# Performance work log

Measured on AMD Instinct MI355X. Metric: run time of the kernel, lower is better.

Reference implementation:

```python
import jax, jax.numpy as jnp
import numpy as np

B, S, D = 1, 4096, 1024
H, HKV, HD = 16, 4, 64          # q heads, kv heads, head dim
ROPE_THETA = 1e6


def setup_inputs() -> dict:
    key = jax.random.key(0)
    k1, k2, k3 = jax.random.split(key, 3)
    x = jax.random.normal(k1, (B, S, D), dtype=jnp.float32)
    # deterministic RoPE tables: pos_cis = exp(i * t * theta^{-2j/hd})
    inv_freq = 1.0 / (ROPE_THETA ** (np.arange(0, HD, 2, dtype=np.float32) / HD))  # [HD//2]
    ang = np.arange(S, dtype=np.float32)[:, None] * inv_freq[None, :]              # [S, HD//2]
    pos_cos = jnp.asarray(np.cos(ang), dtype=jnp.float32)
    pos_sin = jnp.asarray(np.sin(ang), dtype=jnp.float32)
    w_qkv = jax.random.normal(k2, (D, (H + 2 * HKV) * HD), dtype=jnp.float32) * 0.02
    w_o = jax.random.normal(k3, (H * HD, D), dtype=jnp.float32) * 0.02
    return {"x": x, "pos_cos": pos_cos, "pos_sin": pos_sin, "w_qkv": w_qkv, "w_o": w_o}


def _rope(t, pos_cos, pos_sin):
    # t: [B, S, h, HD]; complex pairs are consecutive elements on last dim
    te, to = t[..., 0::2], t[..., 1::2]
    cos = pos_cos[None, :, None, :]
    sin = pos_sin[None, :, None, :]
    oe = te * cos - to * sin
    oo = te * sin + to * cos
    return jnp.stack([oe, oo], axis=-1).reshape(t.shape)


def reference(x, pos_cos, pos_sin, w_qkv, w_o):
    qkv = jnp.einsum("bsd,de->bse", x, w_qkv)  # fused QKV projection
    q = qkv[..., : H * HD].reshape(B, S, H, HD)
    k = qkv[..., H * HD : (H + HKV) * HD].reshape(B, S, HKV, HD)
    v = qkv[..., (H + HKV) * HD :].reshape(B, S, HKV, HD)
    q = _rope(q, pos_cos, pos_sin)
    k = _rope(k, pos_cos, pos_sin)
    # GQA: repeat kv heads to match q heads
    n_rep = H // HKV
    k = jnp.repeat(k, n_rep, axis=2)  # [B, S, H, HD]
    v = jnp.repeat(v, n_rep, axis=2)
    scale = 1.0 / jnp.sqrt(jnp.float32(HD))
    scores = jnp.einsum("bqhd,bkhd->bhqk", q, k) * scale  # [B, H, S, S]
    causal = jnp.tril(jnp.ones((S, S), dtype=bool))
    scores = jnp.where(causal[None, None], scores, jnp.float32(-1e9))
    attn = jax.nn.softmax(scores, axis=-1)
    out = jnp.einsum("bhqk,bkhd->bqhd", attn, v).reshape(B, S, H * HD)
    return jnp.einsum("bse,ed->bsd", out, w_o)
```

## Files before the change

kernel.cpp:

```cpp
#include <hip/hip_runtime.h>

#define S_LEN 4096
#define DMODEL 1024
#define NH 16
#define NKV 4
#define HDIM 64
#define NQKV 1536

typedef __attribute__((ext_vector_type(8))) short bfrag8;
typedef __attribute__((ext_vector_type(4))) float f32x4_t;

__device__ __forceinline__ unsigned short f2bf(float f) {
  unsigned int u = __builtin_bit_cast(unsigned int, f);
  return (unsigned short)((u + 0x7fffu + ((u >> 16) & 1u)) >> 16);
}

__device__ __forceinline__ unsigned int cvtpk_bf16(float lo, float hi) {
  unsigned int r;
  asm("v_cvt_pk_bf16_f32 %0, %1, %2" : "=v"(r) : "v"(lo), "v"(hi));
  return r;
}

__device__ __forceinline__ float fexp2(float x) {
  float r;
  asm("v_exp_f32 %0, %1" : "=v"(r) : "v"(x));
  return r;
}

__device__ __forceinline__ float fmax3(float a, float b, float c) {
  float r;
  asm("v_max3_f32 %0, %1, %2, %3" : "=v"(r) : "v"(a), "v"(b), "v"(c));
  return r;
}

typedef __attribute__((address_space(3))) unsigned char lds_uc;
typedef const __attribute__((address_space(1))) unsigned char glob_uc;
__device__ __forceinline__ void gl16(const void* g, void* l) {
  __builtin_amdgcn_global_load_lds((glob_uc*)g, (lds_uc*)l, 16, 0, 0);
}

__global__ void convert_bf16(const float* __restrict__ in, unsigned short* __restrict__ out, int n) {
  int idx = (blockIdx.x * 256 + threadIdx.x) * 4;
  if (idx < n) {
    float4 v = *reinterpret_cast<const float4*>(in + idx);
    out[idx + 0] = f2bf(v.x);
    out[idx + 1] = f2bf(v.y);
    out[idx + 2] = f2bf(v.z);
    out[idx + 3] = f2bf(v.w);
  }
}

__global__ void transpose_convert(const float* __restrict__ in, int ldin, long in_zstride,
                                  unsigned short* __restrict__ out, int ldout, long out_zstride,
                                  int R, int C) {
  __shared__ float tile[32][33];
  const float* inb = in + (size_t)blockIdx.z * in_zstride;
  unsigned short* outb = out + (size_t)blockIdx.z * out_zstride;
  int c0 = blockIdx.x * 32, r0 = blockIdx.y * 32;
  int tx = threadIdx.x, ty = threadIdx.y;
  for (int i = 0; i < 4; ++i) {
    int r = r0 + ty + i * 8;
    tile[ty + i * 8][tx] = inb[(size_t)r * ldin + c0 + tx];
  }
  __syncthreads();
  for (int i = 0; i < 4; ++i) {
    int c = c0 + ty + i * 8;
    outb[(size_t)c * ldout + r0 + tx] = f2bf(tile[tx][ty + i * 8]);
  }
}

__global__ void rope_kernel(const float* __restrict__ qkv,
                            const float* __restrict__ pcos, const float* __restrict__ psin,
                            unsigned short* __restrict__ Qh, unsigned short* __restrict__ Kh) {
  const float SCL = 0.125f * 1.44269504f;
  int s = blockIdx.x;
  int t = threadIdx.x;
  const float* row = qkv + (size_t)s * NQKV;
  for (int p = t; p < 640; p += 256) {
    int i = p & 31;
    float c = pcos[s * 32 + i], sn = psin[s * 32 + i];
    if (p < 512) {
      int h = p >> 5;
      float te = row[h * 64 + 2 * i], to = row[h * 64 + 2 * i + 1];
      size_t base = ((size_t)h * S_LEN + s) * 64;
      Qh[base + 2 * i]     = f2bf((te * c - to * sn) * SCL);
      Qh[base + 2 * i + 1] = f2bf((te * sn + to * c) * SCL);
    } else {
      int hk = (p - 512) >> 5;
      float te = row[1024 + hk * 64 + 2 * i], to = row[1024 + hk * 64 + 2 * i + 1];
      size_t base = ((size_t)hk * S_LEN + s) * 64;
      Kh[base + 2 * i]     = f2bf(te * c - to * sn);
      Kh[base + 2 * i + 1] = f2bf(te * sn + to * c);
    }
  }
}

__global__ __launch_bounds__(256) void gemm_bf16(
    const unsigned short* __restrict__ A,
    const unsigned short* __restrict__ Bt,
    float* __restrict__ C, int M, int N, int K) {
  __shared__ __align__(16) unsigned short As[128 * 32];
  __shared__ __align__(16) unsigned short Bs[128 * 32];
  int m0 = blockIdx.x * 128, n0 = blockIdx.y * 128;
  int t = threadIdx.x, lane = t & 63, wid = t >> 6;
  int wm = (wid >> 1) * 64, wn = (wid & 1) * 64;
  int fr = lane & 15, kb = lane >> 4;
  int srow = t >> 2, scol = (t & 3) * 8;
  const unsigned short* Ag0 = A + (size_t)(m0 + srow) * K + scol;
  const unsigned short* Ag1 = A + (size_t)(m0 + 64 + srow) * K + scol;
  const unsigned short* Bg0 = Bt + (size_t)(n0 + srow) * K + scol;
  const unsigned short* Bg1 = Bt + (size_t)(n0 + 64 + srow) * K + scol;
  char* AsW0 = (char*)As + wid * 1024;
  char* AsW1 = (char*)As + 4096 + wid * 1024;
  char* BsW0 = (char*)Bs + wid * 1024;
  char* BsW1 = (char*)Bs + 4096 + wid * 1024;

  f32x4_t acc[4][4];
#pragma unroll
  for (int r = 0; r < 4; ++r)
#pragma unroll
    for (int c = 0; c < 4; ++c) acc[r][c] = (f32x4_t){0.f, 0.f, 0.f, 0.f};

  for (int k0 = 0; k0 < K; k0 += 32) {
    __syncthreads();
    gl16(Ag0 + k0, AsW0);
    gl16(Ag1 + k0, AsW1);
    gl16(Bg0 + k0, BsW0);
    gl16(Bg1 + k0, BsW1);
    __syncthreads();
    bfrag8 af[4], bfr[4];
#pragma unroll
    for (int rb = 0; rb < 4; ++rb)
      af[rb] = *reinterpret_cast<const bfrag8*>(&As[(wm + rb * 16 + fr) * 32 + kb * 8]);
#pragma unroll
    for (int cb = 0; cb < 4; ++cb)
      bfr[cb] = *reinterpret_cast<const bfrag8*>(&Bs[(wn + cb * 16 + fr) * 32 + kb * 8]);
#pragma unroll
    for (int rb = 0; rb < 4; ++rb)
#pragma unroll
      for (int cb = 0; cb < 4; ++cb)
        acc[rb][cb] = __builtin_amdgcn_mfma_f32_16x16x32_bf16(af[rb], bfr[cb], acc[rb][cb], 0, 0, 0);
  }
  int rowg = (lane >> 4) * 4, colg = lane & 15;
#pragma unroll
  for (int rb = 0; rb < 4; ++rb)
#pragma unroll
    for (int cb = 0; cb < 4; ++cb)
#pragma unroll
      for (int j = 0; j < 4; ++j) {
        int r = m0 + wm + rb * 16 + rowg + j;
        int c = n0 + wn + cb * 16 + colg;
        C[(size_t)r * N + c] = acc[rb][cb][j];
      }
}

__global__ __launch_bounds__(256) void flash_attn(
    const unsigned short* __restrict__ Qh,
    const unsigned short* __restrict__ Kh,
    const unsigned short* __restrict__ Vt,
    unsigned short* __restrict__ aout) {
  __shared__ __align__(16) char SMEM[18432];
  int bid = blockIdx.x;
  int head = bid & 15, hk = head >> 2;
  int qt = 127 - (bid >> 4);
  int qrow0 = qt * 32;
  int t = threadIdx.x, lane = t & 63, wid = t >> 6;
  int fr = lane & 15, kb = lane >> 4, rloc = kb * 4;
  char* Pw = SMEM + wid * 4096;
  int swz = (fr & 7) << 4;

  const unsigned short* Qbase = Qh + ((size_t)head * S_LEN + qrow0) * 64;
  bfrag8 qf[2][2];
  qf[0][0] = *reinterpret_cast<const bfrag8*>(Qbase + fr * 64 + kb * 8);
  qf[0][1] = *reinterpret_cast<const bfrag8*>(Qbase + fr * 64 + 32 + kb * 8);
  qf[1][0] = *reinterpret_cast<const bfrag8*>(Qbase + (16 + fr) * 64 + kb * 8);
  qf[1][1] = *reinterpret_cast<const bfrag8*>(Qbase + (16 + fr) * 64 + 32 + kb * 8);

  const unsigned short* Kt = Kh + (size_t)hk * S_LEN * 64;
  const unsigned short* Vb = Vt + (size_t)hk * 64 * S_LEN;
  int koff = fr * 64 + kb * 8;
  int voff = fr * S_LEN + kb * 8;

  float m_r[2] = {-1e30f, -1e30f}, l_r[2] = {0.f, 0.f};
  f32x4_t acc[2][4];
#pragma unroll
  for (int g = 0; g < 2; ++g)
#pragma unroll
    for (int dt = 0; dt < 4; ++dt) acc[g][dt] = (f32x4_t){0.f, 0.f, 0.f, 0.f};

  int ntt = (qrow0 + 95) / 64;
  int nf = (qrow0 >= 63) ? ((qrow0 - 63) / 64 + 1) : 0;
  int c0 = (wid * ntt) >> 2, c1 = ((wid + 1) * ntt) >> 2;

  if (c0 < c1) {
    bfrag8 kf[4][2];
    {
      const unsigned short* K0 = Kt + c0 * 64 * 64 + koff;
#pragma unroll
      for (int ct = 0; ct < 4; ++ct) {
        kf[ct][0] = *reinterpret_cast<const bfrag8*>(K0 + ct * 1024);
        kf[ct][1] = *reinterpret_cast<const bfrag8*>(K0 + ct * 1024 + 32);
      }
    }
    for (int kt = c0; kt < c1; ++kt) {
      int kv0 = kt * 64;
      const unsigned short* Vtile = Vb + kv0 + voff;
      bfrag8 vf[2][4];
#pragma unroll
      for (int hh = 0; hh < 2; ++hh)
#pragma unroll
        for (int dt = 0; dt < 4; ++dt)
          vf[hh][dt] = *reinterpret_cast<const bfrag8*>(Vtile + dt * 16 * S_LEN + hh * 32);
      __builtin_amdgcn_sched_barrier(0);
      f32x4_t sc[2][4];
      __builtin_amdgcn_s_setprio(1);
#pragma unroll
      for (int ct = 0; ct < 4; ++ct) {
        f32x4_t z0 = (f32x4_t){0.f, 0.f, 0.f, 0.f};
        z0 = __builtin_amdgcn_mfma_f32_16x16x32_bf16(kf[ct][0], qf[0][0], z0, 0, 0, 0);
        sc[0][ct] = __builtin_amdgcn_mfma_f32_16x16x32_bf16(kf[ct][1], qf[0][1], z0, 0, 0, 0);
        f32x4_t z1 = (f32x4_t){0.f, 0.f, 0.f, 0.f};
        z1 = __builtin_amdgcn_mfma_f32_16x16x32_bf16(kf[ct][0], qf[1][0], z1, 0, 0, 0);
        sc[1][ct] = __builtin_amdgcn_mfma_f32_16x16x32_bf16(kf[ct][1], qf[1][1], z1, 0, 0, 0);
      }
      __builtin_amdgcn_s_setprio(0);
      if (kt + 1 < c1) {
        const unsigned short* Kn = Kt + (kv0 + 64) * 64 + koff;
#pragma unroll
        for (int ct = 0; ct < 4; ++ct) {
          kf[ct][0] = *reinterpret_cast<const bfrag8*>(Kn + ct * 1024);
          kf[ct][1] = *reinterpret_cast<const bfrag8*>(Kn + ct * 1024 + 32);
        }
      }
      __builtin_amdgcn_sched_barrier(0);
      if (kt >= nf) {
#pragma unroll
        for (int g = 0; g < 2; ++g) {
          int grow = qrow0 + g * 16 + fr;
#pragma unroll
          for (int ct = 0; ct < 4; ++ct)
#pragma unroll
            for (int j = 0; j < 4; ++j)
              sc[g][ct][j] = ((kv0 + ct * 16 + kb * 4 + j) <= grow) ? sc[g][ct][j] : -1e30f;
        }
      }
      float pmax[2];
#pragma unroll
      for (int g = 0; g < 2; ++g) {
        float pm = fmax3(sc[g][0][0], sc[g][0][1], sc[g][0][2]);
        pm = fmax3(pm, sc[g][0][3], sc[g][1][0]);
        pm = fmax3(pm, sc[g][1][1], sc[g][1][2]);
        pm = fmax3(pm, sc[g][1][3], sc[g][2][0]);
        pm = fmax3(pm, sc[g][2][1], sc[g][2][2]);
        pm = fmax3(pm, sc[g][2][3], sc[g][3][0]);
        pm = fmax3(pm, sc[g][3][1], sc[g][3][2]);
        pm = fmaxf(pm, sc[g][3][3]);
        pm = fmaxf(pm, __shfl_xor(pm, 16));
        pmax[g] = fmaxf(pm, __shfl_xor(pm, 32));
      }
      bool need = (pmax[0] > m_r[0] + 8.0f) || (pmax[1] > m_r[1] + 8.0f);
      if (__any(need)) {
#pragma unroll
        for (int g = 0; g < 2; ++g) {
          float mnew = fmaxf(m_r[g], pmax[g]);
          float a = fexp2(m_r[g] - mnew);
          l_r[g] *= a;
          m_r[g] = mnew;
#pragma unroll
          for (int j = 0; j < 4; ++j) {
            float aj = __shfl(a, rloc + j);
#pragma unroll
            for (int dt = 0; dt < 4; ++dt) acc[g][dt][j] *= aj;
          }
        }
      }
#pragma unroll
      for (int g = 0; g < 2; ++g) {
        float s = 0.f;
#pragma unroll
        for (int ct = 0; ct < 4; ++ct)
#pragma unroll
          for (int j = 0; j < 4; ++j) {
            float p = fexp2(sc[g][ct][j] - m_r[g]);
            sc[g][ct][j] = p;
            s += p;
          }
        s += __shfl_xor(s, 16);
        s += __shfl_xor(s, 32);
        l_r[g] += s;
      }
#pragma unroll
      for (int g = 0; g < 2; ++g)
#pragma unroll
        for (int ct = 0; ct < 4; ++ct) {
          unsigned int u01 = cvtpk_bf16(sc[g][ct][0], sc[g][ct][1]);
          unsigned int u23 = cvtpk_bf16(sc[g][ct][2], sc[g][ct][3]);
          unsigned long long w = ((unsigned long long)u23 << 32) | u01;
          *reinterpret_cast<unsigned long long*>(
              Pw + (g * 16 + fr) * 128 + ((ct * 32 + kb * 8) ^ swz)) = w;
        }
      __builtin_amdgcn_s_setprio(1);
#pragma unroll
      for (int hh = 0; hh < 2; ++hh) {
        bfrag8 pa0 = *reinterpret_cast<const bfrag8*>(Pw + fr * 128 + ((hh * 64 + kb * 16) ^ swz));
        bfrag8 pa1 = *reinterpret_cast<const bfrag8*>(Pw + (16 + fr) * 128 + ((hh * 64 + kb * 16) ^ swz));
#pragma unroll
        for (int dt = 0; dt < 4; ++dt) {
          acc[0][dt] = __builtin_amdgcn_mfma_f32_16x16x32_bf16(pa0, vf[hh][dt], acc[0][dt], 0, 0, 0);
          acc[1][dt] = __builtin_amdgcn_mfma_f32_16x16x32_bf16(pa1, vf[hh][dt], acc[1][dt], 0, 0, 0);
        }
      }
      __builtin_amdgcn_s_setprio(0);
    }
  }

  float* stgA = (float*)SMEM;
  float* stgB = (float*)(SMEM + 9216);
  __syncthreads();
  if (wid == 1 || wid == 3) {
    float* R = (wid == 1) ? stgA : stgB;
#pragma unroll
    for (int g = 0; g < 2; ++g) {
#pragma unroll
      for (int dt = 0; dt < 4; ++dt)
#pragma unroll
        for (int j = 0; j < 4; ++j)
          R[(g * 16 + dt * 4 + j) * 64 + lane] = acc[g][dt][j];
      R[(32 + g * 2) * 64 + lane] = m_r[g];
      R[(33 + g * 2) * 64 + lane] = l_r[g];
    }
  }
  __syncthreads();
  if (wid == 0 || wid == 2) {
    float* R = (wid == 0) ? stgA : stgB;
#pragma unroll
    for (int g = 0; g < 2; ++g) {
      float mo = R[(32 + g * 2) * 64 + lane], lo = R[(33 + g * 2) * 64 + lane];
      float mm = fmaxf(m_r[g], mo);
      float ca = fexp2(m_r[g] - mm), cb = fexp2(mo - mm);
      l_r[g] = l_r[g] * ca + lo * cb;
      m_r[g] = mm;
#pragma unroll
      for (int j = 0; j < 4; ++j) {
        float caj = __shfl(ca, rloc + j);
        float cbj = __shfl(cb, rloc + j);
#pragma unroll
        for (int dt = 0; dt < 4; ++dt)
          acc[g][dt][j] = acc[g][dt][j] * caj + R[(g * 16 + dt * 4 + j) * 64 + lane] * cbj;
      }
    }
    if (wid == 2) {
#pragma unroll
      for (int g = 0; g < 2; ++g) {
#pragma unroll
        for (int dt = 0; dt < 4; ++dt)
#pragma unroll
          for (int j = 0; j < 4; ++j)
            stgB[(g * 16 + dt * 4 + j) * 64 + lane] = acc[g][dt][j];
        stgB[(32 + g * 2) * 64 + lane] = m_r[g];
        stgB[(33 + g * 2) * 64 + lane] = l_r[g];
      }
    }
  }
  __syncthreads();
  if (wid == 0) {
#pragma unroll
    for (int g = 0; g < 2; ++g) {
      float mo = stgB[(32 + g * 2) * 64 + lane], lo = stgB[(33 + g * 2) * 64 + lane];
      float mm = fmaxf(m_r[g], mo);
      float ca = fexp2(m_r[g] - mm), cb = fexp2(mo - mm);
      l_r[g] = l_r[g] * ca + lo * cb;
#pragma unroll
      for (int j = 0; j < 4; ++j) {
        float caj = __shfl(ca, rloc + j);
        float cbj = __shfl(cb, rloc + j);
#pragma unroll
        for (int dt = 0; dt < 4; ++dt)
          acc[g][dt][j] = acc[g][dt][j] * caj + stgB[(g * 16 + dt * 4 + j) * 64 + lane] * cbj;
      }
    }
#pragma unroll
    for (int g = 0; g < 2; ++g)
#pragma unroll
      for (int j = 0; j < 4; ++j) {
        float lj = __shfl(l_r[g], rloc + j);
        float inv = 1.0f / lj;
        int grow = qrow0 + g * 16 + rloc + j;
#pragma unroll
        for (int dt = 0; dt < 4; ++dt)
          aout[(size_t)grow * (NH * HDIM) + head * 64 + dt * 16 + fr] = f2bf(acc[g][dt][j] * inv);
      }
  }
}

extern "C" void kernel_launch(void* const* d_in, const int* in_sizes, int n_in,
                              void* d_out, int out_size, void* d_ws, size_t ws_size,
                              hipStream_t stream) {
  const float* x    = (const float*)d_in[0];
  const float* pcos = (const float*)d_in[1];
  const float* psin = (const float*)d_in[2];
  const float* wqkv = (const float*)d_in[3];
  const float* wo   = (const float*)d_in[4];
  float* out = (float*)d_out;

  char* ws = (char*)d_ws;
  unsigned short* xb    = (unsigned short*)ws;  ws += (size_t)S_LEN * DMODEL * 2;
  unsigned short* wqkvT = (unsigned short*)ws;  ws += (size_t)NQKV * DMODEL * 2;
  unsigned short* woT   = (unsigned short*)ws;  ws += (size_t)DMODEL * DMODEL * 2;
  float*          qkv   = (float*)ws;           ws += (size_t)S_LEN * NQKV * 4;
  unsigned short* Qh    = (unsigned short*)ws;  ws += (size_t)NH * S_LEN * HDIM * 2;
  unsigned short* Kh    = (unsigned short*)ws;  ws += (size_t)NKV * S_LEN * HDIM * 2;
  unsigned short* Vt    = (unsigned short*)ws;  ws += (size_t)NKV * HDIM * S_LEN * 2;
  unsigned short* aoutb = (unsigned short*)ws;  ws += (size_t)S_LEN * NH * HDIM * 2;

  convert_bf16<<<(S_LEN * DMODEL) / (256 * 4), 256, 0, stream>>>(x, xb, S_LEN * DMODEL);
  transpose_convert<<<dim3(NQKV / 32, DMODEL / 32, 1), dim3(32, 8), 0, stream>>>(
      wqkv, NQKV, 0, wqkvT, DMODEL, 0, DMODEL, NQKV);
  transpose_convert<<<dim3(DMODEL / 32, DMODEL / 32, 1), dim3(32, 8), 0, stream>>>(
      wo, DMODEL, 0, woT, DMODEL, 0, DMODEL, DMODEL);
  gemm_bf16<<<dim3(S_LEN / 128, NQKV / 128), 256, 0, stream>>>(xb, wqkvT, qkv, S_LEN, NQKV, DMODEL);
  rope_kernel<<<S_LEN, 256, 0, stream>>>(qkv, pcos, psin, Qh, Kh);
  transpose_convert<<<dim3(HDIM / 32, S_LEN / 32, NKV), dim3(32, 8), 0, stream>>>(
      qkv + 1280, NQKV, 64, Vt, S_LEN, (long)HDIM * S_LEN, S_LEN, HDIM);
  flash_attn<<<dim3(2048), 256, 0, stream>>>(Qh, Kh, Vt, aoutb);
  gemm_bf16<<<dim3(S_LEN / 128, DMODEL / 128), 256, 0, stream>>>(aoutb, woT, out, S_LEN, DMODEL, DMODEL);
}
```

Baseline: 204.1 us.

## Split flash-attention KV range across eight waves with tree merge

```diff
diff --git a/kernel.cpp b/kernel.cpp
--- a/kernel.cpp
+++ b/kernel.cpp
@@ -154,12 +154,12 @@
       }
 }
 
-__global__ __launch_bounds__(256) void flash_attn(
+__global__ __launch_bounds__(512) void flash_attn(
     const unsigned short* __restrict__ Qh,
     const unsigned short* __restrict__ Kh,
     const unsigned short* __restrict__ Vt,
     unsigned short* __restrict__ aout) {
-  __shared__ __align__(16) char SMEM[18432];
+  __shared__ __align__(16) char SMEM[32768 + 2048];
   int bid = blockIdx.x;
   int head = bid & 15, hk = head >> 2;
   int qt = 127 - (bid >> 4);
@@ -167,6 +167,7 @@
   int t = threadIdx.x, lane = t & 63, wid = t >> 6;
   int fr = lane & 15, kb = lane >> 4, rloc = kb * 4;
   char* Pw = SMEM + wid * 4096;
+  float* mlp = (float*)(SMEM + 32768);
   int swz = (fr & 7) << 4;
 
   const unsigned short* Qbase = Qh + ((size_t)head * S_LEN + qrow0) * 64;
@@ -190,7 +191,7 @@
 
   int ntt = (qrow0 + 95) / 64;
   int nf = (qrow0 >= 63) ? ((qrow0 - 63) / 64 + 1) : 0;
-  int c0 = (wid * ntt) >> 2, c1 = ((wid + 1) * ntt) >> 2;
+  int c0 = (wid * ntt) >> 3, c1 = ((wid + 1) * ntt) >> 3;
 
   if (c0 < c1) {
     bfrag8 kf[4][2];
@@ -314,71 +315,52 @@
     }
   }
 
-  float* stgA = (float*)SMEM;
-  float* stgB = (float*)(SMEM + 9216);
-  __syncthreads();
-  if (wid == 1 || wid == 3) {
-    float* R = (wid == 1) ? stgA : stgB;
-#pragma unroll
-    for (int g = 0; g < 2; ++g) {
-#pragma unroll
-      for (int dt = 0; dt < 4; ++dt)
-#pragma unroll
-        for (int j = 0; j < 4; ++j)
-          R[(g * 16 + dt * 4 + j) * 64 + lane] = acc[g][dt][j];
-      R[(32 + g * 2) * 64 + lane] = m_r[g];
-      R[(33 + g * 2) * 64 + lane] = l_r[g];
-    }
-  }
-  __syncthreads();
-  if (wid == 0 || wid == 2) {
-    float* R = (wid == 0) ? stgA : stgB;
-#pragma unroll
-    for (int g = 0; g < 2; ++g) {
-      float mo = R[(32 + g * 2) * 64 + lane], lo = R[(33 + g * 2) * 64 + lane];
-      float mm = fmaxf(m_r[g], mo);
-      float ca = fexp2(m_r[g] - mm), cb = fexp2(mo - mm);
-      l_r[g] = l_r[g] * ca + lo * cb;
-      m_r[g] = mm;
-#pragma unroll
-      for (int j = 0; j < 4; ++j) {
-        float caj = __shfl(ca, rloc + j);
-        float cbj = __shfl(cb, rloc + j);
-#pragma unroll
-        for (int dt = 0; dt < 4; ++dt)
-          acc[g][dt][j] = acc[g][dt][j] * caj + R[(g * 16 + dt * 4 + j) * 64 + lane] * cbj;
-      }
-    }
-    if (wid == 2) {
-#pragma unroll
-      for (int g = 0; g < 2; ++g) {
-#pragma unroll
-        for (int dt = 0; dt < 4; ++dt)
-#pragma unroll
-          for (int j = 0; j < 4; ++j)
-            stgB[(g * 16 + dt * 4 + j) * 64 + lane] = acc[g][dt][j];
-        stgB[(32 + g * 2) * 64 + lane] = m_r[g];
-        stgB[(33 + g * 2) * 64 + lane] = l_r[g];
-      }
-    }
-  }
+#define ML(w, g, which, row) mlp[(((w) * 2 + (g)) * 2 + (which)) * 16 + (row)]
+#define STORE_STATE(Rp)                                                   \
+  {                                                                       \
+    float* R = (Rp);                                                      \
+    _Pragma("unroll") for (int g = 0; g < 2; ++g) {                       \
+      _Pragma("unroll") for (int dt = 0; dt < 4; ++dt)                    \
+        _Pragma("unroll") for (int j = 0; j < 4; ++j)                     \
+          R[(g * 16 + dt * 4 + j) * 64 + lane] = acc[g][dt][j];           \
+      if (lane < 16) {                                                    \
+        ML(wid, g, 0, lane) = m_r[g];                                     \
+        ML(wid, g, 1, lane) = l_r[g];                                     \
+      }                                                                   \
+    }                                                                     \
+  }
+#define MERGE_STATE(Rp, wsrc)                                             \
+  {                                                                       \
+    float* R = (Rp);                                                      \
+    _Pragma("unroll") for (int g = 0; g < 2; ++g) {                       \
+      float mo = ML((wsrc), g, 0, fr), lo = ML((wsrc), g, 1, fr);         \
+      float mm = fmaxf(m_r[g], mo);                                       \
+      float ca = fexp2(m_r[g] - mm), cb = fexp2(mo - mm);                 \
+      l_r[g] = l_r[g] * ca + lo * cb;                                     \
+      m_r[g] = mm;                                                        \
+      _Pragma("unroll") for (int j = 0; j < 4; ++j) {                     \
+        float caj = __shfl(ca, rloc + j);                                 \
+        float cbj = __shfl(cb, rloc + j);                                 \
+        _Pragma("unroll") for (int dt = 0; dt < 4; ++dt)                  \
+          acc[g][dt][j] = acc[g][dt][j] * caj +                           \
+                          R[(g * 16 + dt * 4 + j) * 64 + lane] * cbj;     \
+      }                                                                   \
+    }                                                                     \
+  }
+
+  __syncthreads();
+  if (wid & 1) STORE_STATE((float*)(SMEM + (wid >> 1) * 8192));
+  __syncthreads();
+  if (!(wid & 1)) MERGE_STATE((float*)(SMEM + (wid >> 1) * 8192), wid + 1);
+  __syncthreads();
+  if (wid == 2 || wid == 6) STORE_STATE((float*)(SMEM + (wid >> 2) * 8192));
+  __syncthreads();
+  if (wid == 0 || wid == 4) MERGE_STATE((float*)(SMEM + (wid >> 2) * 8192), wid + 2);
+  __syncthreads();
+  if (wid == 4) STORE_STATE((float*)SMEM);
   __syncthreads();
   if (wid == 0) {
-#pragma unroll
-    for (int g = 0; g < 2; ++g) {
-      float mo = stgB[(32 + g * 2) * 64 + lane], lo = stgB[(33 + g * 2) * 64 + lane];
-      float mm = fmaxf(m_r[g], mo);
-      float ca = fexp2(m_r[g] - mm), cb = fexp2(mo - mm);
-      l_r[g] = l_r[g] * ca + lo * cb;
-#pragma unroll
-      for (int j = 0; j < 4; ++j) {
-        float caj = __shfl(ca, rloc + j);
-        float cbj = __shfl(cb, rloc + j);
-#pragma unroll
-        for (int dt = 0; dt < 4; ++dt)
-          acc[g][dt][j] = acc[g][dt][j] * caj + stgB[(g * 16 + dt * 4 + j) * 64 + lane] * cbj;
-      }
-    }
+    MERGE_STATE((float*)SMEM, 4);
 #pragma unroll
     for (int g = 0; g < 2; ++g)
 #pragma unroll
@@ -391,6 +373,9 @@
           aout[(size_t)grow * (NH * HDIM) + head * 64 + dt * 16 + fr] = f2bf(acc[g][dt][j] * inv);
       }
   }
+#undef ML
+#undef STORE_STATE
+#undef MERGE_STATE
 }
 
 extern "C" void kernel_launch(void* const* d_in, const int* in_sizes, int n_in,
@@ -422,6 +407,6 @@
   rope_kernel<<<S_LEN, 256, 0, stream>>>(qkv, pcos, psin, Qh, Kh);
   transpose_convert<<<dim3(HDIM / 32, S_LEN / 32, NKV), dim3(32, 8), 0, stream>>>(
       qkv + 1280, NQKV, 64, Vt, S_LEN, (long)HDIM * S_LEN, S_LEN, HDIM);
-  flash_attn<<<dim3(2048), 256, 0, stream>>>(Qh, Kh, Vt, aoutb);
+  flash_attn<<<dim3(2048), 512, 0, stream>>>(Qh, Kh, Vt, aoutb);
   gemm_bf16<<<dim3(S_LEN / 128, DMODEL / 128), 256, 0, stream>>>(aoutb, woT, out, S_LEN, DMODEL, DMODEL);
 }
```

Result: slower. 235.4 us (+15.4%).

## Split long causal KV ranges across two blocks and merge partials

Applied to the files above, without the earlier changes.

```diff
diff --git a/kernel.cpp b/kernel.cpp
--- a/kernel.cpp
+++ b/kernel.cpp
@@ -158,12 +158,20 @@
     const unsigned short* __restrict__ Qh,
     const unsigned short* __restrict__ Kh,
     const unsigned short* __restrict__ Vt,
-    unsigned short* __restrict__ aout) {
+    float* __restrict__ partial,
+    float* __restrict__ mlb) {
   __shared__ __align__(16) char SMEM[18432];
   int bid = blockIdx.x;
   int head = bid & 15, hk = head >> 2;
-  int qt = 127 - (bid >> 4);
+  int rest = bid >> 4;
+  int cs = rest & 1;
+  int qt = 127 - (rest >> 1);
   int qrow0 = qt * 32;
+  int ntt = (qrow0 + 95) / 64;
+  if (cs == 1 && ntt <= 32) return;
+  int base_t = cs * 32;
+  int hi_t = min(ntt, base_t + 32);
+  int len = hi_t - base_t;
   int t = threadIdx.x, lane = t & 63, wid = t >> 6;
   int fr = lane & 15, kb = lane >> 4, rloc = kb * 4;
   char* Pw = SMEM + wid * 4096;
@@ -188,9 +196,8 @@
 #pragma unroll
     for (int dt = 0; dt < 4; ++dt) acc[g][dt] = (f32x4_t){0.f, 0.f, 0.f, 0.f};
 
-  int ntt = (qrow0 + 95) / 64;
   int nf = (qrow0 >= 63) ? ((qrow0 - 63) / 64 + 1) : 0;
-  int c0 = (wid * ntt) >> 2, c1 = ((wid + 1) * ntt) >> 2;
+  int c0 = base_t + ((wid * len) >> 2), c1 = base_t + (((wid + 1) * len) >> 2);
 
   if (c0 < c1) {
     bfrag8 kf[4][2];
@@ -370,6 +377,7 @@
       float mm = fmaxf(m_r[g], mo);
       float ca = fexp2(m_r[g] - mm), cb = fexp2(mo - mm);
       l_r[g] = l_r[g] * ca + lo * cb;
+      m_r[g] = mm;
 #pragma unroll
       for (int j = 0; j < 4; ++j) {
         float caj = __shfl(ca, rloc + j);
@@ -379,18 +387,56 @@
           acc[g][dt][j] = acc[g][dt][j] * caj + stgB[(g * 16 + dt * 4 + j) * 64 + lane] * cbj;
       }
     }
+    size_t pbase = ((size_t)(head * 2 + cs) * S_LEN + qrow0);
 #pragma unroll
     for (int g = 0; g < 2; ++g)
 #pragma unroll
       for (int j = 0; j < 4; ++j) {
-        float lj = __shfl(l_r[g], rloc + j);
-        float inv = 1.0f / lj;
-        int grow = qrow0 + g * 16 + rloc + j;
+        int r = g * 16 + rloc + j;
 #pragma unroll
         for (int dt = 0; dt < 4; ++dt)
-          aout[(size_t)grow * (NH * HDIM) + head * 64 + dt * 16 + fr] = f2bf(acc[g][dt][j] * inv);
-      }
-  }
+          partial[(pbase + r) * 64 + dt * 16 + fr] = acc[g][dt][j];
+      }
+    if (lane < 16) {
+#pragma unroll
+      for (int g = 0; g < 2; ++g) {
+        mlb[(pbase + g * 16 + lane) * 2 + 0] = m_r[g];
+        mlb[(pbase + g * 16 + lane) * 2 + 1] = l_r[g];
+      }
+    }
+  }
+}
+
+__global__ __launch_bounds__(256) void merge_attn(
+    const float* __restrict__ partial, const float* __restrict__ mlb,
+    unsigned short* __restrict__ aout) {
+  int id = blockIdx.x * 256 + threadIdx.x;
+  int c8 = (id & 7) * 8;
+  int s = (id >> 3) & 4095;
+  int h = id >> 15;
+  size_t b0 = (size_t)(h * 2) * S_LEN + s;
+  float m0 = mlb[b0 * 2], l0 = mlb[b0 * 2 + 1];
+  const float4* P0 = reinterpret_cast<const float4*>(partial + b0 * 64 + c8);
+  float4 a0 = P0[0], a1 = P0[1];
+  float o[8] = {a0.x, a0.y, a0.z, a0.w, a1.x, a1.y, a1.z, a1.w};
+  float inv;
+  if (s >= 2048) {
+    size_t b1 = b0 + S_LEN;
+    float m1 = mlb[b1 * 2], l1 = mlb[b1 * 2 + 1];
+    float mm = fmaxf(m0, m1);
+    float w0 = fexp2(m0 - mm), w1 = fexp2(m1 - mm);
+    const float4* P1 = reinterpret_cast<const float4*>(partial + b1 * 64 + c8);
+    float4 c0v = P1[0], c1v = P1[1];
+    float p1[8] = {c0v.x, c0v.y, c0v.z, c0v.w, c1v.x, c1v.y, c1v.z, c1v.w};
+#pragma unroll
+    for (int k = 0; k < 8; ++k) o[k] = o[k] * w0 + p1[k] * w1;
+    inv = 1.0f / (l0 * w0 + l1 * w1);
+  } else {
+    inv = 1.0f / l0;
+  }
+  unsigned short* dst = aout + (size_t)s * (NH * HDIM) + h * 64 + c8;
+#pragma unroll
+  for (int k = 0; k < 8; ++k) dst[k] = f2bf(o[k] * inv);
 }
 
 extern "C" void kernel_launch(void* const* d_in, const int* in_sizes, int n_in,
@@ -404,14 +450,16 @@
   float* out = (float*)d_out;
 
   char* ws = (char*)d_ws;
+  float*          qkv   = (float*)ws;           ws += (size_t)S_LEN * NQKV * 4;
   unsigned short* xb    = (unsigned short*)ws;  ws += (size_t)S_LEN * DMODEL * 2;
   unsigned short* wqkvT = (unsigned short*)ws;  ws += (size_t)NQKV * DMODEL * 2;
   unsigned short* woT   = (unsigned short*)ws;  ws += (size_t)DMODEL * DMODEL * 2;
-  float*          qkv   = (float*)ws;           ws += (size_t)S_LEN * NQKV * 4;
   unsigned short* Qh    = (unsigned short*)ws;  ws += (size_t)NH * S_LEN * HDIM * 2;
   unsigned short* Kh    = (unsigned short*)ws;  ws += (size_t)NKV * S_LEN * HDIM * 2;
   unsigned short* Vt    = (unsigned short*)ws;  ws += (size_t)NKV * HDIM * S_LEN * 2;
   unsigned short* aoutb = (unsigned short*)ws;  ws += (size_t)S_LEN * NH * HDIM * 2;
+  float* partial = qkv;
+  float* mlbuf   = (float*)wqkvT;
 
   convert_bf16<<<(S_LEN * DMODEL) / (256 * 4), 256, 0, stream>>>(x, xb, S_LEN * DMODEL);
   transpose_convert<<<dim3(NQKV / 32, DMODEL / 32, 1), dim3(32, 8), 0, stream>>>(
@@ -422,6 +470,7 @@
   rope_kernel<<<S_LEN, 256, 0, stream>>>(qkv, pcos, psin, Qh, Kh);
   transpose_convert<<<dim3(HDIM / 32, S_LEN / 32, NKV), dim3(32, 8), 0, stream>>>(
       qkv + 1280, NQKV, 64, Vt, S_LEN, (long)HDIM * S_LEN, S_LEN, HDIM);
-  flash_attn<<<dim3(2048), 256, 0, stream>>>(Qh, Kh, Vt, aoutb);
+  flash_attn<<<dim3(4096), 256, 0, stream>>>(Qh, Kh, Vt, partial, mlbuf);
+  merge_attn<<<dim3((NH * S_LEN * 8) / 256), 256, 0, stream>>>(partial, mlbuf, aoutb);
   gemm_bf16<<<dim3(S_LEN / 128, DMODEL / 128), 256, 0, stream>>>(aoutb, woT, out, S_LEN, DMODEL, DMODEL);
 }
```

Result: slower. 268.6 us (+31.6%).
